# Performance work log

Hardware: AMD Instinct MI355X
Metric: run time of the kernel (lower is better)

## Reference

```python
import jax, jax.numpy as jnp
import numpy as np

N, L, S, D, H = 4, 8192, 8192, 256, 8
DH = D // H  # 32
EPS_ATTN = 1e-6
EPS_LN = 1e-5


def setup_inputs() -> dict:
    key = jax.random.key(0)
    ks = jax.random.split(key, 8)
    w = lambda k, sh: jax.random.normal(k, sh, jnp.float32) * 0.02
    return {
        "x": jax.random.normal(ks[0], (N, L, D), jnp.float32),
        "source": jax.random.normal(ks[1], (N, S, D), jnp.float32),
        "Wq": w(ks[2], (D, D)),
        "Wk": w(ks[3], (D, D)),
        "Wv": w(ks[4], (D, D)),
        "Wm": w(ks[5], (D, D)),
        "W1": w(ks[6], (2 * D, 2 * D)),
        "W2": w(ks[7], (2 * D, D)),
        "g1": jnp.ones((D,), jnp.float32),
        "b1": jnp.zeros((D,), jnp.float32),
        "g2": jnp.ones((D,), jnp.float32),
        "b2": jnp.zeros((D,), jnp.float32),
    }


def _layernorm(x, g, b):
    m = jnp.mean(x, axis=-1, keepdims=True)
    v = jnp.var(x, axis=-1, keepdims=True)
    return (x - m) * jax.lax.rsqrt(v + EPS_LN) * g + b


def reference(x, source, Wq, Wk, Wv, Wm, W1, W2, g1, b1, g2, b2):
    bs = x.shape[0]
    # QKV projections (bias=False), split heads -> [N, L/S, H, DH]
    q = (x @ Wq).reshape(bs, -1, H, DH)
    k = (source @ Wk).reshape(bs, -1, H, DH)
    v = (source @ Wv).reshape(bs, -1, H, DH)
    # elu+1 feature map (linear attention, LoFTR-style)
    Q = jax.nn.elu(q) + 1.0
    K = jax.nn.elu(k) + 1.0
    v_len = v.shape[1]
    vals = v / v_len
    KV = jnp.einsum("nshd,nshv->nhdv", K, vals)  # [N, H, DH, DH]
    Z = 1.0 / (jnp.einsum("nlhd,nhd->nlh", Q, K.sum(axis=1)) + EPS_ATTN)
    msg = jnp.einsum("nlhd,nhdv,nlh->nlhv", Q, KV, Z) * v_len  # [N, L, H, DH]
    # merge heads + LN
    msg = msg.reshape(bs, -1, H * DH) @ Wm
    msg = _layernorm(msg, g1, b1)
    # concat-MLP with LeakyReLU(0.1)
    h = jnp.concatenate([x, msg], axis=2) @ W1
    h = jnp.where(h >= 0, h, 0.1 * h)
    msg = h @ W2
    msg = _layernorm(msg, g2, b2)
    return x + msg
```

## Files before the change

kernel.cpp:

```cpp
#include <hip/hip_runtime.h>

typedef __bf16 bf16;
typedef __bf16 bf16x4 __attribute__((ext_vector_type(4)));
typedef __bf16 bf16x8 __attribute__((ext_vector_type(8)));
typedef float f32x4 __attribute__((ext_vector_type(4)));

__device__ __forceinline__ float apply_epi(float v, int epi) {
  if (epi == 1) return v > 0.f ? v + 1.f : __expf(v);
  if (epi == 2) return v >= 0.f ? v : 0.1f * v;
  return v;
}

__device__ __forceinline__ void g2l16(const bf16* gp, bf16* lp) {
  __builtin_amdgcn_global_load_lds(
      (const __attribute__((address_space(1))) void*)gp,
      (__attribute__((address_space(3))) void*)lp, 16, 0, 0);
}

__device__ __forceinline__ bool is_f32(const unsigned* w) { return w[0] == 0x3F800000u; }

struct TransArgs {
  const void* src[6];
  bf16* dst[6];
  int R[6], C[6], t0[6];
};

__global__ __launch_bounds__(256) void prep_kernel(
    const void* __restrict__ xin, const void* __restrict__ sin,
    bf16* __restrict__ bx, bf16* __restrict__ bs,
    TransArgs ta, const unsigned* __restrict__ g1w) {
  const bool f32 = is_f32(g1w);
  if (blockIdx.x < 8192) {
    const void* s;
    bf16* d;
    size_t i;
    if (blockIdx.x < 4096) {
      s = xin; d = bx; i = (size_t)blockIdx.x * 2048 + threadIdx.x * 8;
    } else {
      s = sin; d = bs; i = (size_t)(blockIdx.x - 4096) * 2048 + threadIdx.x * 8;
    }
    if (f32) {
      f32x4 lo = *(const f32x4*)((const float*)s + i);
      f32x4 hi = *(const f32x4*)((const float*)s + i + 4);
      bf16x8 t;
      t[0] = (bf16)lo[0]; t[1] = (bf16)lo[1]; t[2] = (bf16)lo[2]; t[3] = (bf16)lo[3];
      t[4] = (bf16)hi[0]; t[5] = (bf16)hi[1]; t[6] = (bf16)hi[2]; t[7] = (bf16)hi[3];
      *(bf16x8*)(d + i) = t;
    } else {
      *(bf16x8*)(d + i) = *(const bf16x8*)((const bf16*)s + i);
    }
    return;
  }
  __shared__ bf16 tile[32][33];
  int bid = blockIdx.x - 8192;
  int si = 0;
#pragma unroll
  for (int i = 1; i < 6; ++i)
    if (bid >= ta.t0[i]) si = i;
  const void* srcv = ta.src[si];
  bf16* dst = ta.dst[si];
  int R = ta.R[si], Cc = ta.C[si];
  int lt = bid - ta.t0[si];
  int tpr = Cc >> 5;
  int tr = lt / tpr, tc = lt % tpr;
  int tx = threadIdx.x & 31, ty0 = threadIdx.x >> 5;
#pragma unroll
  for (int i = 0; i < 4; ++i) {
    int ty = ty0 + i * 8;
    size_t idx = (size_t)(tr * 32 + ty) * Cc + tc * 32 + tx;
    tile[ty][tx] = f32 ? (bf16)((const float*)srcv)[idx] : ((const bf16*)srcv)[idx];
  }
  __syncthreads();
#pragma unroll
  for (int i = 0; i < 4; ++i) {
    int ty = ty0 + i * 8;
    dst[(size_t)(tc * 32 + ty) * R + tr * 32 + tx] = tile[tx][ty];
  }
}

__device__ __forceinline__ void gemm_core32(
    const bf16* __restrict__ A, const bf16* __restrict__ A2, int ldA,
    const bf16* __restrict__ Bt, int Kk, int m0, int n0,
    bf16 (&As)[3][4096], bf16 (&Bs)[3][4096], f32x4 (&acc)[4][2], int tid) {
  const int wave = tid >> 6, lane = tid & 63;
  const int wm = (wave >> 2) * 64, wn = (wave & 3) * 32;
  const int q = lane >> 4, mr = lane & 15;
  const int kTiles = Kk >> 5;
  const int rr = tid >> 2, pp = tid & 3;
  const int gg = pp ^ ((rr >> 1) & 3);

  auto stage = [&](int kt, int buf) {
    int kcol = kt * 32;
    const bf16* Ab = A;
    if (A2 && kcol >= 256) { Ab = A2; kcol -= 256; }
    g2l16(Ab + (size_t)(m0 + rr) * ldA + kcol + gg * 8, &As[buf][tid * 8]);
    g2l16(Bt + (size_t)(n0 + rr) * Kk + kt * 32 + gg * 8, &Bs[buf][tid * 8]);
  };
  auto compute = [&](int buf) {
    bf16x8 af[4], bfv[2];
#pragma unroll
    for (int mi = 0; mi < 4; ++mi) {
      int r = wm + mi * 16 + mr;
      af[mi] = *(const bf16x8*)&As[buf][r * 32 + (q ^ ((r >> 1) & 3)) * 8];
    }
#pragma unroll
    for (int ni = 0; ni < 2; ++ni) {
      int r = wn + ni * 16 + mr;
      bfv[ni] = *(const bf16x8*)&Bs[buf][r * 32 + (q ^ ((r >> 1) & 3)) * 8];
    }
#pragma unroll
    for (int mi = 0; mi < 4; ++mi)
#pragma unroll
      for (int ni = 0; ni < 2; ++ni)
        acc[mi][ni] = __builtin_amdgcn_mfma_f32_16x16x32_bf16(af[mi], bfv[ni], acc[mi][ni], 0, 0, 0);
  };

  stage(0, 0);
  stage(1, 1);
  asm volatile("s_waitcnt vmcnt(2)\n\ts_barrier" ::: "memory");
  int kt = 0;
  for (; kt < kTiles - 2; ++kt) {
    stage(kt + 2, (kt + 2) % 3);
    compute(kt % 3);
    asm volatile("s_waitcnt vmcnt(2) lgkmcnt(0)\n\ts_barrier" ::: "memory");
  }
  compute(kt % 3);
  asm volatile("s_waitcnt vmcnt(0) lgkmcnt(0)\n\ts_barrier" ::: "memory");
  compute((kt + 1) % 3);
}

__global__ __launch_bounds__(512, 4) void gemm_qkv(
    const bf16* __restrict__ Ax, const bf16* __restrict__ As_,
    const bf16* __restrict__ BtQ, const bf16* __restrict__ BtKV,
    bf16* __restrict__ Cq, bf16* __restrict__ Ck, bf16* __restrict__ Cv) {
  __shared__ bf16 AsL[3][4096];
  __shared__ bf16 BsL[3][4096];
  const int tid = threadIdx.x;
  const int lin = blockIdx.x;
  const int u = (lin & 7) * 192 + (lin >> 3);

  const bf16* Ap; const bf16* Btp; bf16* Cp; int ep, m0, n0, cbase;
  if (u < 512) {
    int mb = u >> 1, nb = u & 1;
    Ap = Ax; Btp = BtQ; Cp = Cq; ep = 1;
    m0 = mb * 128; n0 = nb * 128; cbase = n0;
  } else {
    int local = u - 512;
    int mb = local >> 2, nb = local & 3;
    Ap = As_; Btp = BtKV;
    m0 = mb * 128; n0 = nb * 128;
    if (nb < 2) { Cp = Ck; ep = 1; cbase = n0; }
    else        { Cp = Cv; ep = 0; cbase = n0 - 256; }
  }

  f32x4 acc[4][2];
#pragma unroll
  for (int i = 0; i < 4; ++i)
#pragma unroll
    for (int j = 0; j < 2; ++j) acc[i][j] = (f32x4){0.f, 0.f, 0.f, 0.f};

  gemm_core32(Ap, nullptr, 256, Btp, 256, m0, n0, AsL, BsL, acc, tid);

  const int wave = tid >> 6, lane = tid & 63;
  const int wm = (wave >> 2) * 64, wn = (wave & 3) * 32;
  const int q = lane >> 4, mr = lane & 15;
#pragma unroll
  for (int mi = 0; mi < 4; ++mi)
#pragma unroll
    for (int ni = 0; ni < 2; ++ni)
#pragma unroll
      for (int r4 = 0; r4 < 4; ++r4) {
        int row = m0 + wm + mi * 16 + q * 4 + r4;
        int cn = cbase + wn + ni * 16 + mr;
        Cp[(size_t)row * 256 + cn] = (bf16)apply_epi(acc[mi][ni][r4], ep);
      }
}

__global__ __launch_bounds__(512, 4) void gemm_rt(
    const bf16* __restrict__ A, const bf16* __restrict__ A2, int ldA,
    const bf16* __restrict__ Bt, bf16* __restrict__ C, int Nn, int Kk, int epi) {
  __shared__ bf16 AsL[3][4096];
  __shared__ bf16 BsL[3][4096];
  const int tid = threadIdx.x;

  const int nwg = gridDim.x * gridDim.y;
  const int lin = blockIdx.y * gridDim.x + blockIdx.x;
  const int cpx = nwg >> 3;
  const int u = (lin & 7) * cpx + (lin >> 3);
  const int ny = gridDim.y;
  const int mb = u / ny, nb = u - mb * ny;
  const int m0 = mb * 128;
  const int n0 = nb * 128;

  f32x4 acc[4][2];
#pragma unroll
  for (int i = 0; i < 4; ++i)
#pragma unroll
    for (int j = 0; j < 2; ++j) acc[i][j] = (f32x4){0.f, 0.f, 0.f, 0.f};

  gemm_core32(A, A2, ldA, Bt, Kk, m0, n0, AsL, BsL, acc, tid);

  const int wave = tid >> 6, lane = tid & 63;
  const int wm = (wave >> 2) * 64, wn = (wave & 3) * 32;
  const int q = lane >> 4, mr = lane & 15;
#pragma unroll
  for (int mi = 0; mi < 4; ++mi)
#pragma unroll
    for (int ni = 0; ni < 2; ++ni)
#pragma unroll
      for (int r4 = 0; r4 < 4; ++r4) {
        int row = m0 + wm + mi * 16 + q * 4 + r4;
        int cn = n0 + wn + ni * 16 + mr;
        C[(size_t)row * Nn + cn] = (bf16)apply_epi(acc[mi][ni][r4], epi);
      }
}

#define KVCH 256
__global__ __launch_bounds__(256) void kv_kernel(
    const bf16* __restrict__ Kf, const bf16* __restrict__ V,
    float* __restrict__ partial, float* __restrict__ pk) {
  __shared__ bf16 Ks[KVCH][32];
  __shared__ bf16 Vs[KVCH][32];
  const int cb = blockIdx.x, h = blockIdx.y, n = blockIdx.z;
  const int tid = threadIdx.x;
  const int wave = tid >> 6, lane = tid & 63;
  const int d0 = (lane & 7) * 4, dv0 = (lane >> 3) * 4;
  const int s0 = cb * KVCH;
#pragma unroll
  for (int rd = 0; rd < 4; ++rd) {
    int rr = rd * 64 + (tid >> 2), pp = tid & 3;
    size_t g = ((size_t)(n * 8192 + s0 + rr)) * 256 + h * 32 + pp * 8;
    *(bf16x8*)&Ks[rr][pp * 8] = *(const bf16x8*)(Kf + g);
    *(bf16x8*)&Vs[rr][pp * 8] = *(const bf16x8*)(V + g);
  }
  __syncthreads();
  float acc[4][4] = {};
  float ks4[4] = {};
#pragma unroll 4
  for (int si = 0; si < 64; ++si) {
    int s = wave * 64 + si;
    bf16x4 k4 = *(const bf16x4*)&Ks[s][d0];
    bf16x4 v4 = *(const bf16x4*)&Vs[s][dv0];
    float kf[4] = {(float)k4[0], (float)k4[1], (float)k4[2], (float)k4[3]};
    float vf[4] = {(float)v4[0], (float)v4[1], (float)v4[2], (float)v4[3]};
#pragma unroll
    for (int vi = 0; vi < 4; ++vi)
#pragma unroll
      for (int di = 0; di < 4; ++di) acc[vi][di] = fmaf(vf[vi], kf[di], acc[vi][di]);
#pragma unroll
    for (int di = 0; di < 4; ++di) ks4[di] += kf[di];
  }
  __syncthreads();
  float* red = (float*)&Ks[0][0];
  float* ksr = (float*)&Vs[0][0];
#pragma unroll
  for (int vi = 0; vi < 4; ++vi)
#pragma unroll
    for (int di = 0; di < 4; ++di)
      red[wave * 1024 + (dv0 + vi) * 32 + d0 + di] = acc[vi][di];
  if (dv0 == 0) {
#pragma unroll
    for (int di = 0; di < 4; ++di) ksr[wave * 32 + d0 + di] = ks4[di];
  }
  __syncthreads();
  const size_t slot = (size_t)(n * 8 + h) * 32 + cb;
  f32x4 s4 = {0.f, 0.f, 0.f, 0.f};
#pragma unroll
  for (int w = 0; w < 4; ++w) s4 += *(const f32x4*)&red[w * 1024 + tid * 4];
  *(f32x4*)&partial[slot * 1024 + tid * 4] = s4;
  if (tid < 32) {
    float ss = 0.f;
#pragma unroll
    for (int w = 0; w < 4; ++w) ss += ksr[w * 32 + tid];
    pk[slot * 32 + tid] = ss;
  }
}

__global__ __launch_bounds__(256) void kv_reduce(
    const float* __restrict__ partial, const float* __restrict__ pk,
    float* __restrict__ kv_acc, float* __restrict__ ksum) {
  const int b = blockIdx.x;
  const int t = threadIdx.x;
  f32x4 s4 = {0.f, 0.f, 0.f, 0.f};
  for (int c = 0; c < 32; ++c)
    s4 += *(const f32x4*)&partial[((size_t)b * 32 + c) * 1024 + t * 4];
  *(f32x4*)&kv_acc[(size_t)b * 1024 + t * 4] = s4;
  if (t < 32) {
    float ss = 0.f;
    for (int c = 0; c < 32; ++c) ss += pk[((size_t)b * 32 + c) * 32 + t];
    ksum[(size_t)b * 32 + t] = ss;
  }
}

__global__ __launch_bounds__(256) void msg_kernel(
    const bf16* __restrict__ Q, const float* __restrict__ kv_acc,
    const float* __restrict__ ksum, bf16* __restrict__ msg) {
  __shared__ bf16 kvt[8][32][32];
  __shared__ float ksl[8][32];
  __shared__ float zl[8][128];
  int tid = threadIdx.x;
  int row0 = blockIdx.x * 128;
  int n = row0 >> 13;
  const float* kvb = kv_acc + (size_t)n * 8192;
  for (int i = tid; i < 8192; i += 256) ((bf16*)kvt)[i] = (bf16)kvb[i];
  ((float*)ksl)[tid] = ksum[(size_t)n * 256 + tid];
  __syncthreads();
  int r = tid & 127, hg = tid >> 7;
  const bf16* qrow = Q + (size_t)(row0 + r) * 256;
#pragma unroll
  for (int hh = 0; hh < 4; ++hh) {
    int h = hg * 4 + hh;
    float dot = 0.f;
#pragma unroll
    for (int d = 0; d < 32; ++d) dot = fmaf((float)qrow[h * 32 + d], ksl[h][d], dot);
    zl[h][r] = 1.f / (dot + 1e-6f);
  }
  __syncthreads();
  int wave = tid >> 6, lane = tid & 63, q = lane >> 4, mr = lane & 15;
  f32x4 zero = {0.f, 0.f, 0.f, 0.f};
  for (int h = 0; h < 8; ++h) {
    bf16x8 b0 = *(const bf16x8*)&kvt[h][mr][q * 8];
    bf16x8 b1 = *(const bf16x8*)&kvt[h][16 + mr][q * 8];
#pragma unroll
    for (int mi = 0; mi < 2; ++mi) {
      int arow = wave * 32 + mi * 16 + mr;
      bf16x8 a = *(const bf16x8*)(Q + (size_t)(row0 + arow) * 256 + h * 32 + q * 8);
      f32x4 c0 = __builtin_amdgcn_mfma_f32_16x16x32_bf16(a, b0, zero, 0, 0, 0);
      f32x4 c1 = __builtin_amdgcn_mfma_f32_16x16x32_bf16(a, b1, zero, 0, 0, 0);
#pragma unroll
      for (int r4 = 0; r4 < 4; ++r4) {
        int orow = wave * 32 + mi * 16 + q * 4 + r4;
        float z = zl[h][orow];
        size_t ob = (size_t)(row0 + orow) * 256 + h * 32;
        msg[ob + mr] = (bf16)(c0[r4] * z);
        msg[ob + 16 + mr] = (bf16)(c1[r4] * z);
      }
    }
  }
}

__global__ __launch_bounds__(256) void ln_kernel(
    const bf16* __restrict__ in, const void* __restrict__ g, const void* __restrict__ b,
    const void* __restrict__ resid, void* __restrict__ outp,
    const unsigned* __restrict__ g1w, int ioDual) {
  const bool gbF32 = is_f32(g1w);
  const bool ioF32 = ioDual && gbF32;
  int wave = threadIdx.x >> 6, lane = threadIdx.x & 63;
  size_t row = (size_t)blockIdx.x * 4 + wave;
  int c = lane * 4;
  bf16x4 v = *(const bf16x4*)(in + row * 256 + c);
  float x0 = (float)v[0], x1 = (float)v[1], x2 = (float)v[2], x3 = (float)v[3];
  float s = x0 + x1 + x2 + x3;
  float sq = x0 * x0 + x1 * x1 + x2 * x2 + x3 * x3;
#pragma unroll
  for (int o = 32; o > 0; o >>= 1) {
    s += __shfl_xor(s, o);
    sq += __shfl_xor(sq, o);
  }
  float mean = s * (1.f / 256.f);
  float var = sq * (1.f / 256.f) - mean * mean;
  float rstd = rsqrtf(var + 1e-5f);
  float g0, g1v, g2v, g3, b0, b1v, b2v, b3;
  if (gbF32) {
    f32x4 gv = *(const f32x4*)((const float*)g + c);
    f32x4 bv = *(const f32x4*)((const float*)b + c);
    g0 = gv[0]; g1v = gv[1]; g2v = gv[2]; g3 = gv[3];
    b0 = bv[0]; b1v = bv[1]; b2v = bv[2]; b3 = bv[3];
  } else {
    bf16x4 gv = *(const bf16x4*)((const bf16*)g + c);
    bf16x4 bv = *(const bf16x4*)((const bf16*)b + c);
    g0 = (float)gv[0]; g1v = (float)gv[1]; g2v = (float)gv[2]; g3 = (float)gv[3];
    b0 = (float)bv[0]; b1v = (float)bv[1]; b2v = (float)bv[2]; b3 = (float)bv[3];
  }
  float y0 = (x0 - mean) * rstd * g0 + b0;
  float y1 = (x1 - mean) * rstd * g1v + b1v;
  float y2 = (x2 - mean) * rstd * g2v + b2v;
  float y3 = (x3 - mean) * rstd * g3 + b3;
  if (resid) {
    if (ioF32) {
      f32x4 rv = *(const f32x4*)((const float*)resid + row * 256 + c);
      y0 += rv[0]; y1 += rv[1]; y2 += rv[2]; y3 += rv[3];
    } else {
      bf16x4 rv = *(const bf16x4*)((const bf16*)resid + row * 256 + c);
      y0 += (float)rv[0]; y1 += (float)rv[1]; y2 += (float)rv[2]; y3 += (float)rv[3];
    }
  }
  if (ioF32) {
    f32x4 o4 = {y0, y1, y2, y3};
    *(f32x4*)((float*)outp + row * 256 + c) = o4;
  } else {
    bf16x4 o4;
    o4[0] = (bf16)y0; o4[1] = (bf16)y1; o4[2] = (bf16)y2; o4[3] = (bf16)y3;
    *(bf16x4*)((bf16*)outp + row * 256 + c) = o4;
  }
}

extern "C" void kernel_launch(void* const* d_in, const int* in_sizes, int n_in,
                              void* d_out, int out_size, void* d_ws, size_t ws_size,
                              hipStream_t stream) {
  const void* x   = d_in[0];
  const void* src = d_in[1];
  const void* Wq  = d_in[2];
  const void* Wk  = d_in[3];
  const void* Wv  = d_in[4];
  const void* Wm  = d_in[5];
  const void* W1  = d_in[6];
  const void* W2  = d_in[7];
  const void* g1  = d_in[8];
  const void* b1  = d_in[9];
  const void* g2  = d_in[10];
  const void* b2  = d_in[11];

  char* ws = (char*)d_ws;
  bf16* bufA = (bf16*)(ws);
  bf16* bufB = (bf16*)(ws + ((size_t)16 << 20));
  bf16* bufC = (bf16*)(ws + ((size_t)32 << 20));
  bf16* WqT  = (bf16*)(ws + ((size_t)48 << 20));
  bf16* WkvT = WqT + 65536;
  bf16* WmT  = WkvT + 131072;
  bf16* W1T  = WmT + 65536;
  bf16* W2T  = W1T + 262144;
  float* kv_acc = (float*)(ws + ((size_t)50 << 20));
  float* ksum = kv_acc + 32768;
  float* partial = (float*)(ws + ((size_t)51 << 20));
  float* pk = (float*)(ws + ((size_t)55 << 20));
  bf16* bufX = (bf16*)d_out;
  bf16* bufS = bufX + 8388608;

  TransArgs ta;
  ta.src[0] = Wq; ta.src[1] = Wk; ta.src[2] = Wv; ta.src[3] = Wm; ta.src[4] = W1; ta.src[5] = W2;
  ta.dst[0] = WqT; ta.dst[1] = WkvT; ta.dst[2] = WkvT + 65536; ta.dst[3] = WmT; ta.dst[4] = W1T; ta.dst[5] = W2T;
  ta.R[0] = 256; ta.R[1] = 256; ta.R[2] = 256; ta.R[3] = 256; ta.R[4] = 512; ta.R[5] = 512;
  ta.C[0] = 256; ta.C[1] = 256; ta.C[2] = 256; ta.C[3] = 256; ta.C[4] = 512; ta.C[5] = 256;
  ta.t0[0] = 0; ta.t0[1] = 64; ta.t0[2] = 128; ta.t0[3] = 192; ta.t0[4] = 256; ta.t0[5] = 512;
  prep_kernel<<<dim3(8832), dim3(256), 0, stream>>>(x, src, bufX, bufS, ta, (const unsigned*)g1);

  gemm_qkv<<<dim3(1536), dim3(512), 0, stream>>>(bufX, bufS, WqT, WkvT, bufA, bufB, bufC);

  kv_kernel<<<dim3(32, 8, 4), dim3(256), 0, stream>>>(bufB, bufC, partial, pk);
  kv_reduce<<<dim3(32), dim3(256), 0, stream>>>(partial, pk, kv_acc, ksum);

  msg_kernel<<<dim3(256), dim3(256), 0, stream>>>(bufA, kv_acc, ksum, bufB);

  gemm_rt<<<dim3(256, 2), dim3(512), 0, stream>>>(bufB, nullptr, 256, WmT, bufA, 256, 256, 0);

  ln_kernel<<<dim3(8192), dim3(256), 0, stream>>>(bufA, g1, b1, nullptr, bufC,
                                                  (const unsigned*)g1, 0);

  gemm_rt<<<dim3(256, 4), dim3(512), 0, stream>>>(bufX, bufC, 256, W1T, bufA, 512, 512, 2);

  gemm_rt<<<dim3(256, 2), dim3(512), 0, stream>>>(bufA, nullptr, 512, W2T, bufC, 256, 512, 0);

  ln_kernel<<<dim3(8192), dim3(256), 0, stream>>>(bufC, g2, b2, x, d_out,
                                                  (const unsigned*)g1, 1);
}
```

Before: 257.8 us.

## Fuse LayerNorm into full-row GEMM epilogue for merge and MLP output

Adds a gemm_ln kernel in which each workgroup computes a full 128x256 output tile, so it owns whole rows. Row mean and variance are reduced with shuffles and a small LDS scratch, then LayerNorm (and the residual add for the final stage) is applied before storing. This replaces two GEMM+LN kernel pairs and removes the bf16 intermediate write and re-read plus two launches. In exchange the grid shrinks to 256 workgroups, each holding more accumulators and a larger B tile in LDS, which may lower occupancy and parallelism.

```diff
diff --git a/kernel.cpp b/kernel.cpp
--- a/kernel.cpp
+++ b/kernel.cpp
@@ -78,7 +78,7 @@
   }
 }
 
-__device__ __forceinline__ void gemm_core32(
+__device__ __forceinline__ void gemm_core_n(
     const bf16* __restrict__ A, const bf16* __restrict__ A2, int ldA,
     const bf16* __restrict__ Bt, int Kk, int m0, int n0,
     bf16 (&As)[3][4096], bf16 (&Bs)[3][4096], f32x4 (&acc)[4][2], int tid) {
@@ -159,7 +159,7 @@
 #pragma unroll
     for (int j = 0; j < 2; ++j) acc[i][j] = (f32x4){0.f, 0.f, 0.f, 0.f};
 
-  gemm_core32(Ap, nullptr, 256, Btp, 256, m0, n0, AsL, BsL, acc, tid);
+  gemm_core_n(Ap, nullptr, 256, Btp, 256, m0, n0, AsL, BsL, acc, tid);
 
   const int wave = tid >> 6, lane = tid & 63;
   const int wm = (wave >> 2) * 64, wn = (wave & 3) * 32;
@@ -198,7 +198,7 @@
 #pragma unroll
     for (int j = 0; j < 2; ++j) acc[i][j] = (f32x4){0.f, 0.f, 0.f, 0.f};
 
-  gemm_core32(A, A2, ldA, Bt, Kk, m0, n0, AsL, BsL, acc, tid);
+  gemm_core_n(A, A2, ldA, Bt, Kk, m0, n0, AsL, BsL, acc, tid);
 
   const int wave = tid >> 6, lane = tid & 63;
   const int wm = (wave >> 2) * 64, wn = (wave & 3) * 32;
@@ -213,6 +213,140 @@
         int cn = n0 + wn + ni * 16 + mr;
         C[(size_t)row * Nn + cn] = (bf16)apply_epi(acc[mi][ni][r4], epi);
       }
+}
+
+__global__ __launch_bounds__(512, 4) void gemm_ln(
+    const bf16* __restrict__ A, int ldA, const bf16* __restrict__ Bt, int Kk,
+    const void* __restrict__ gptr, const void* __restrict__ bptr,
+    const void* __restrict__ resid, void* __restrict__ outp, bf16* __restrict__ Cout,
+    const unsigned* __restrict__ g1w, int mode) {
+  __shared__ bf16 AsL[3][4096];
+  __shared__ bf16 BsL[3][8192];
+  const int tid = threadIdx.x;
+  const int lin = blockIdx.x;
+  const int u = (lin & 7) * 32 + (lin >> 3);
+  const int m0 = u * 128;
+
+  const int wave = tid >> 6, lane = tid & 63;
+  const int wm = (wave >> 2) * 64;
+  const int wn = (wave & 3) * 64;
+  const int q = lane >> 4, mr = lane & 15;
+  const int wq = wave & 3;
+  const int kTiles = Kk >> 5;
+
+  f32x4 acc[4][4];
+#pragma unroll
+  for (int i = 0; i < 4; ++i)
+#pragma unroll
+    for (int j = 0; j < 4; ++j) acc[i][j] = (f32x4){0.f, 0.f, 0.f, 0.f};
+
+  {
+    const int rrA = tid >> 2, ppA = tid & 3;
+    const int ggA = ppA ^ ((rrA >> 1) & 3);
+    auto stage = [&](int kt, int buf) {
+      int kcol = kt * 32;
+      g2l16(A + (size_t)(m0 + rrA) * ldA + kcol + ggA * 8, &AsL[buf][tid * 8]);
+#pragma unroll
+      for (int it = 0; it < 2; ++it) {
+        int id = it * 512 + tid;
+        int rr = id >> 2, pp = id & 3, gg = pp ^ ((rr >> 1) & 3);
+        g2l16(Bt + (size_t)rr * Kk + kt * 32 + gg * 8, &BsL[buf][id * 8]);
+      }
+    };
+    auto compute = [&](int buf) {
+      bf16x8 af[4], bfv[4];
+#pragma unroll
+      for (int mi = 0; mi < 4; ++mi) {
+        int r = wm + mi * 16 + mr;
+        af[mi] = *(const bf16x8*)&AsL[buf][r * 32 + (q ^ ((r >> 1) & 3)) * 8];
+      }
+#pragma unroll
+      for (int ni = 0; ni < 4; ++ni) {
+        int r = wn + ni * 16 + mr;
+        bfv[ni] = *(const bf16x8*)&BsL[buf][r * 32 + (q ^ ((r >> 1) & 3)) * 8];
+      }
+#pragma unroll
+      for (int mi = 0; mi < 4; ++mi)
+#pragma unroll
+        for (int ni = 0; ni < 4; ++ni)
+          acc[mi][ni] = __builtin_amdgcn_mfma_f32_16x16x32_bf16(af[mi], bfv[ni], acc[mi][ni], 0, 0, 0);
+    };
+    stage(0, 0);
+    stage(1, 1);
+    asm volatile("s_waitcnt vmcnt(3)\n\ts_barrier" ::: "memory");
+    int kt = 0;
+    for (; kt < kTiles - 2; ++kt) {
+      stage(kt + 2, (kt + 2) % 3);
+      compute(kt % 3);
+      asm volatile("s_waitcnt vmcnt(3) lgkmcnt(0)\n\ts_barrier" ::: "memory");
+    }
+    compute(kt % 3);
+    asm volatile("s_waitcnt vmcnt(0) lgkmcnt(0)\n\ts_barrier" ::: "memory");
+    compute((kt + 1) % 3);
+  }
+
+  const bool f32io = is_f32(g1w);
+  float* scr = (float*)&AsL[0][0];
+  __syncthreads();
+#pragma unroll
+  for (int mi = 0; mi < 4; ++mi)
+#pragma unroll
+    for (int r4 = 0; r4 < 4; ++r4) {
+      float v0 = acc[mi][0][r4], v1 = acc[mi][1][r4], v2 = acc[mi][2][r4], v3 = acc[mi][3][r4];
+      float s = v0 + v1 + v2 + v3;
+      float sq = v0 * v0 + v1 * v1 + v2 * v2 + v3 * v3;
+#pragma unroll
+      for (int o = 1; o < 16; o <<= 1) {
+        s += __shfl_xor(s, o);
+        sq += __shfl_xor(sq, o);
+      }
+      if (mr == 0) {
+        int row = wm + mi * 16 + q * 4 + r4;
+        scr[row * 8 + wq * 2 + 0] = s;
+        scr[row * 8 + wq * 2 + 1] = sq;
+      }
+    }
+  __syncthreads();
+
+  float gv[4], bv[4];
+#pragma unroll
+  for (int ni = 0; ni < 4; ++ni) {
+    int col = wn + ni * 16 + mr;
+    if (f32io) {
+      gv[ni] = ((const float*)gptr)[col];
+      bv[ni] = ((const float*)bptr)[col];
+    } else {
+      gv[ni] = (float)((const bf16*)gptr)[col];
+      bv[ni] = (float)((const bf16*)bptr)[col];
+    }
+  }
+
+#pragma unroll
+  for (int mi = 0; mi < 4; ++mi)
+#pragma unroll
+    for (int r4 = 0; r4 < 4; ++r4) {
+      int row = wm + mi * 16 + q * 4 + r4;
+      float S = scr[row * 8 + 0] + scr[row * 8 + 2] + scr[row * 8 + 4] + scr[row * 8 + 6];
+      float SQ = scr[row * 8 + 1] + scr[row * 8 + 3] + scr[row * 8 + 5] + scr[row * 8 + 7];
+      float mean = S * (1.f / 256.f);
+      float var = SQ * (1.f / 256.f) - mean * mean;
+      float rstd = rsqrtf(var + 1e-5f);
+#pragma unroll
+      for (int ni = 0; ni < 4; ++ni) {
+        int col = wn + ni * 16 + mr;
+        float y = (acc[mi][ni][r4] - mean) * rstd * gv[ni] + bv[ni];
+        size_t off = (size_t)(m0 + row) * 256 + col;
+        if (mode == 0) {
+          Cout[off] = (bf16)y;
+        } else {
+          if (f32io) {
+            ((float*)outp)[off] = y + ((const float*)resid)[off];
+          } else {
+            ((bf16*)outp)[off] = (bf16)(y + (float)((const bf16*)resid)[off]);
+          }
+        }
+      }
+    }
 }
 
 #define KVCH 256
@@ -336,62 +470,6 @@
         msg[ob + 16 + mr] = (bf16)(c1[r4] * z);
       }
     }
-  }
-}
-
-__global__ __launch_bounds__(256) void ln_kernel(
-    const bf16* __restrict__ in, const void* __restrict__ g, const void* __restrict__ b,
-    const void* __restrict__ resid, void* __restrict__ outp,
-    const unsigned* __restrict__ g1w, int ioDual) {
-  const bool gbF32 = is_f32(g1w);
-  const bool ioF32 = ioDual && gbF32;
-  int wave = threadIdx.x >> 6, lane = threadIdx.x & 63;
-  size_t row = (size_t)blockIdx.x * 4 + wave;
-  int c = lane * 4;
-  bf16x4 v = *(const bf16x4*)(in + row * 256 + c);
-  float x0 = (float)v[0], x1 = (float)v[1], x2 = (float)v[2], x3 = (float)v[3];
-  float s = x0 + x1 + x2 + x3;
-  float sq = x0 * x0 + x1 * x1 + x2 * x2 + x3 * x3;
-#pragma unroll
-  for (int o = 32; o > 0; o >>= 1) {
-    s += __shfl_xor(s, o);
-    sq += __shfl_xor(sq, o);
-  }
-  float mean = s * (1.f / 256.f);
-  float var = sq * (1.f / 256.f) - mean * mean;
-  float rstd = rsqrtf(var + 1e-5f);
-  float g0, g1v, g2v, g3, b0, b1v, b2v, b3;
-  if (gbF32) {
-    f32x4 gv = *(const f32x4*)((const float*)g + c);
-    f32x4 bv = *(const f32x4*)((const float*)b + c);
-    g0 = gv[0]; g1v = gv[1]; g2v = gv[2]; g3 = gv[3];
-    b0 = bv[0]; b1v = bv[1]; b2v = bv[2]; b3 = bv[3];
-  } else {
-    bf16x4 gv = *(const bf16x4*)((const bf16*)g + c);
-    bf16x4 bv = *(const bf16x4*)((const bf16*)b + c);
-    g0 = (float)gv[0]; g1v = (float)gv[1]; g2v = (float)gv[2]; g3 = (float)gv[3];
-    b0 = (float)bv[0]; b1v = (float)bv[1]; b2v = (float)bv[2]; b3 = (float)bv[3];
-  }
-  float y0 = (x0 - mean) * rstd * g0 + b0;
-  float y1 = (x1 - mean) * rstd * g1v + b1v;
-  float y2 = (x2 - mean) * rstd * g2v + b2v;
-  float y3 = (x3 - mean) * rstd * g3 + b3;
-  if (resid) {
-    if (ioF32) {
-      f32x4 rv = *(const f32x4*)((const float*)resid + row * 256 + c);
-      y0 += rv[0]; y1 += rv[1]; y2 += rv[2]; y3 += rv[3];
-    } else {
-      bf16x4 rv = *(const bf16x4*)((const bf16*)resid + row * 256 + c);
-      y0 += (float)rv[0]; y1 += (float)rv[1]; y2 += (float)rv[2]; y3 += (float)rv[3];
-    }
-  }
-  if (ioF32) {
-    f32x4 o4 = {y0, y1, y2, y3};
-    *(f32x4*)((float*)outp + row * 256 + c) = o4;
-  } else {
-    bf16x4 o4;
-    o4[0] = (bf16)y0; o4[1] = (bf16)y1; o4[2] = (bf16)y2; o4[3] = (bf16)y3;
-    *(bf16x4*)((bf16*)outp + row * 256 + c) = o4;
   }
 }
 
@@ -442,15 +520,11 @@
 
   msg_kernel<<<dim3(256), dim3(256), 0, stream>>>(bufA, kv_acc, ksum, bufB);
 
-  gemm_rt<<<dim3(256, 2), dim3(512), 0, stream>>>(bufB, nullptr, 256, WmT, bufA, 256, 256, 0);
-
-  ln_kernel<<<dim3(8192), dim3(256), 0, stream>>>(bufA, g1, b1, nullptr, bufC,
-                                                  (const unsigned*)g1, 0);
+  gemm_ln<<<dim3(256), dim3(512), 0, stream>>>(bufB, 256, WmT, 256, g1, b1,
+                                               nullptr, nullptr, bufC, (const unsigned*)g1, 0);
 
   gemm_rt<<<dim3(256, 4), dim3(512), 0, stream>>>(bufX, bufC, 256, W1T, bufA, 512, 512, 2);
 
-  gemm_rt<<<dim3(256, 2), dim3(512), 0, stream>>>(bufA, nullptr, 512, W2T, bufC, 256, 512, 0);
-
-  ln_kernel<<<dim3(8192), dim3(256), 0, stream>>>(bufC, g2, b2, x, d_out,
-                                                  (const unsigned*)g1, 1);
-}
+  gemm_ln<<<dim3(256), dim3(512), 0, stream>>>(bufA, 512, W2T, 512, g2, b2,
+                                               x, d_out, nullptr, (const unsigned*)g1, 1);
+}
```

Result: slower. 271.7 us (+5.4%).
